# Optimization experiments

Measured on AMD Instinct MI355X. Metric: run time of the kernel, lower is better.

## Reference

```python
import jax, jax.numpy as jnp
import numpy as np

NUM_HEADS = 12
CF = 2            # compression_factor
DEPTH = 3
BLOCK_DEPTH = 2
TOTAL_DEPTH_M1 = 14 - 1


def setup_inputs() -> dict:
    key = jax.random.key(0)
    k1, k2, k3, k4 = jax.random.split(key, 4)
    B, N, C = 64, 577, 768
    x = jax.random.normal(k1, (B, N, C), dtype=jnp.float32)
    qkv_w = jax.random.normal(k2, (3 * C, C), dtype=jnp.float32) * (C ** -0.5)
    proj_w = jax.random.normal(k3, (C, C), dtype=jnp.float32) * (C ** -0.5)
    proj_b = jax.random.normal(k4, (C,), dtype=jnp.float32) * 0.02
    return {"x": x, "qkv_w": qkv_w, "proj_w": proj_w, "proj_b": proj_b}


def _attn_branch(xh, qkv_w, proj_w, proj_b, zero_small):
    Bh, N, C = xh.shape
    H = NUM_HEADS
    D = C // H
    scale = D ** -0.5
    # qkv projection (no bias), split into q,k,v of shape [Bh, H, N, D]
    qkv = jnp.einsum('bnc,oc->bno', xh, qkv_w)  # [Bh, N, 3C]
    qkv = qkv.reshape(Bh, N, 3, H, D).transpose(2, 0, 3, 1, 4)  # [3, Bh, H, N, D]
    if zero_small:
        # statically zero compressed heads in q, k, v (as the torch in-place write does)
        qkv = qkv.at[:, :, H // CF:].set(0.0)
    q, k, v = qkv[0], qkv[1], qkv[2]
    attn = jnp.einsum('bhnd,bhmd->bhnm', q, k) * scale
    attn = jax.nn.softmax(attn, axis=-1)
    out = jnp.einsum('bhnm,bhmd->bhnd', attn, v)
    out = out.transpose(0, 2, 1, 3).reshape(Bh, N, C)
    out = jnp.einsum('bnc,oc->bno', out, proj_w) + proj_b
    if zero_small:
        out = out.at[:, :, C // CF:].set(0.0)
    return out


def reference(x, qkv_w, proj_w, proj_b):
    B = x.shape[0]
    x_large = _attn_branch(x[:B // 2], qkv_w, proj_w, proj_b, zero_small=False)
    if BLOCK_DEPTH <= DEPTH <= TOTAL_DEPTH_M1 - BLOCK_DEPTH:
        x_small = _attn_branch(x[B // 2:], qkv_w, proj_w, proj_b, zero_small=True)
        return jnp.concatenate((x_large, x_small), axis=0)
    return jnp.concatenate((x_large, x_large), axis=0)
```

## Files before the change

### kernel.cpp

```cpp
#include <hip/hip_runtime.h>

#define BATCH 64
#define SEQ   577
#define CDIM  768
#define NH    12
#define HD    64
#define MROWS (BATCH * SEQ)
#define KDIM  768
#define QKV_N (3 * CDIM)
#define NPAD  640
#define TQ    128
#define PS    40
#define OS    72
#define DEAD_ROW0 18560

typedef short bf16x8 __attribute__((ext_vector_type(8)));
typedef float f32x4  __attribute__((ext_vector_type(4)));

__device__ __forceinline__ unsigned short f2bf(float f) {
  unsigned int u = __float_as_uint(f);
  u += 0x7fffu + ((u >> 16) & 1u);
  return (unsigned short)(u >> 16);
}

__device__ __forceinline__ void async_ld16(const unsigned short* g, unsigned short* l) {
  __builtin_amdgcn_global_load_lds((const __attribute__((address_space(1))) void*)g,
                                   (__attribute__((address_space(3))) void*)l, 16, 0, 0);
}

__global__ __launch_bounds__(256) void cvt_bf16(const float* __restrict__ in,
                                                unsigned short* __restrict__ out, int n4) {
  int i = blockIdx.x * 256 + threadIdx.x;
  if (i < n4) {
    float4 f = ((const float4*)in)[i];
    ushort4 o = make_ushort4(f2bf(f.x), f2bf(f.y), f2bf(f.z), f2bf(f.w));
    ((ushort4*)out)[i] = o;
  }
}

__global__ __launch_bounds__(256) void gemm_qkv(
    const unsigned short* __restrict__ A,
    const unsigned short* __restrict__ Bm,
    unsigned short* __restrict__ qb,
    unsigned short* __restrict__ kb,
    unsigned short* __restrict__ vb) {
  const int row0 = blockIdx.x * 128;
  const int col0 = blockIdx.y * 128;
  if (row0 >= DEAD_ROW0 && (col0 % CDIM) >= (CDIM / 2)) return;

  __shared__ unsigned short sA[128 * 32];
  __shared__ unsigned short sB[128 * 32];
  const int tid = threadIdx.x;
  const int w = tid >> 6, lane = tid & 63;
  const int quad = lane >> 4, l16 = lane & 15;
  const int wr = w >> 1, wc = w & 1;

  f32x4 acc[4][4] = {};

  for (int kt = 0; kt < KDIM; kt += 32) {
    __syncthreads();
    #pragma unroll
    for (int c = 0; c < 2; c++) {
      int i = tid + c * 256;
      int r = i >> 2, k8 = (i & 3) * 8;
      int ibase = (tid & ~63) + c * 256;
      int gr = row0 + r; if (gr >= MROWS) gr = MROWS - 1;
      async_ld16(A + gr * KDIM + kt + k8, sA + ibase * 8);
      int gc = col0 + r;
      async_ld16(Bm + gc * KDIM + kt + k8, sB + ibase * 8);
    }
    __syncthreads();

    bf16x8 af[4], bfv[4];
    #pragma unroll
    for (int i = 0; i < 4; i++)
      af[i] = *(const bf16x8*)&sA[(wr * 64 + i * 16 + l16) * 32 + quad * 8];
    #pragma unroll
    for (int j = 0; j < 4; j++)
      bfv[j] = *(const bf16x8*)&sB[(wc * 64 + j * 16 + l16) * 32 + quad * 8];
    #pragma unroll
    for (int i = 0; i < 4; i++)
      #pragma unroll
      for (int j = 0; j < 4; j++)
        acc[i][j] = __builtin_amdgcn_mfma_f32_16x16x32_bf16(af[i], bfv[j], acc[i][j], 0, 0, 0);
  }

  #pragma unroll
  for (int i = 0; i < 4; i++) {
    int mbase = row0 + wr * 64 + i * 16 + quad * 4;
    #pragma unroll
    for (int j = 0; j < 4; j++) {
      int col = col0 + wc * 64 + j * 16 + l16;
      int three = col / CDIM;
      int rem = col - three * CDIM;
      int h = rem >> 6, d = rem & 63;
      unsigned short* dst = (three == 0) ? qb : (three == 1) ? kb : vb;
      float sc = (three == 0) ? 0.180336878f : 1.0f;
      #pragma unroll
      for (int r = 0; r < 4; r++) {
        int m = mbase + r;
        if (m < MROWS) {
          int b = m / SEQ;
          int n = m - b * SEQ;
          dst[(((b * NH + h) * SEQ + n) << 6) + d] = f2bf(acc[i][j][r] * sc);
        }
      }
    }
  }
}

__global__ __launch_bounds__(512) void transpose_v(
    const unsigned short* __restrict__ v,
    unsigned short* __restrict__ vt) {
  const int bh = blockIdx.y;
  const int b = bh / NH, h = bh - b * NH;
  if (b >= 32 && h >= 6) return;
  const int t = blockIdx.x;
  const int tid = threadIdx.x;
  const int w = tid >> 6, lane = tid & 63;
  int n = t * 64 + lane;
  bf16x8 vv = {};
  if (n < SEQ)
    vv = *(const bf16x8*)&v[(size_t)bh * (SEQ * HD) + n * HD + w * 8];
  unsigned short* dst = vt + (size_t)bh * (HD * NPAD) + (w * 8) * NPAD + t * 64 + lane;
  #pragma unroll
  for (int j = 0; j < 8; j++)
    dst[j * NPAD] = ((const unsigned short*)&vv)[j];
}

__global__ __launch_bounds__(256, 4) void flash_attn(
    const unsigned short* __restrict__ q,
    const unsigned short* __restrict__ k,
    const unsigned short* __restrict__ vt,
    unsigned short* __restrict__ attn) {
  const int id = blockIdx.x;
  const int bh8 = id / 40;
  const int rem = id - bh8 * 40;
  const int qt = rem >> 3;
  const int bh = bh8 * 8 + (rem & 7);
  const int b = bh / NH, h = bh - b * NH;
  const int tid = threadIdx.x;
  const int w = tid >> 6, lane = tid & 63;
  const int quad = lane >> 4, l16 = lane & 15;

  if (b >= 32 && h >= 6) {
    for (int it = tid; it < TQ * 8; it += 256) {
      int r = it >> 3, c8 = (it & 7) * 8;
      int n = qt * TQ + r;
      if (n < SEQ)
        *(int4*)&attn[(b * SEQ + n) * CDIM + h * 64 + c8] = make_int4(0, 0, 0, 0);
    }
    return;
  }

  __shared__ unsigned short sK[2 * 64 * 32];
  __shared__ unsigned short sVt[2 * 64 * 32];
  __shared__ unsigned short sP[4][64 * PS];

  const unsigned short* qbase = q + (size_t)bh * (SEQ * HD);
  const unsigned short* kbase = k + (size_t)bh * (SEQ * HD);
  const unsigned short* vtbase = vt + (size_t)bh * (HD * NPAD);

  bf16x8 aq[2][2];
  #pragma unroll
  for (int g = 0; g < 2; g++) {
    int qr = qt * TQ + w * 32 + g * 16 + l16;
    if (qr > SEQ - 1) qr = SEQ - 1;
    aq[g][0] = *(const bf16x8*)&qbase[qr * HD + quad * 8];
    aq[g][1] = *(const bf16x8*)&qbase[qr * HD + 32 + quad * 8];
  }

  f32x4 oacc[2][4] = {};
  f32x4 lacc[2] = {};

  const short ONE = (short)0x3F80;

  for (int t = 0; t < 10; t++) {
    __syncthreads();
    #pragma unroll
    for (int c = 0; c < 2; c++) {
      int rI = tid >> 2, c4 = tid & 3;
      int base = c * 2048 + (tid & ~63) * 8;
      int kr = t * 64 + rI; if (kr > SEQ - 1) kr = SEQ - 1;
      async_ld16(kbase + kr * HD + c * 32 + c4 * 8, sK + base);
      async_ld16(vtbase + rI * NPAD + t * 64 + c * 32 + c4 * 8, sVt + base);
    }
    __syncthreads();

    bf16x8 bk[4][2];
    #pragma unroll
    for (int nt = 0; nt < 4; nt++) {
      bk[nt][0] = *(const bf16x8*)&sK[0 * 2048 + (nt * 16 + l16) * 32 + quad * 8];
      bk[nt][1] = *(const bf16x8*)&sK[1 * 2048 + (nt * 16 + l16) * 32 + quad * 8];
    }

    bf16x8 ones0, ones1;
    if (t < 9) {
      #pragma unroll
      for (int j = 0; j < 8; j++) { ones0[j] = ONE; ones1[j] = ONE; }
    } else {
      bf16x8 z = {};
      ones0 = z; ones1 = z;
      ones0[0] = (quad == 0) ? ONE : (short)0;
    }

    #pragma unroll
    for (int g = 0; g < 2; g++) {
      f32x4 s[4];
      #pragma unroll
      for (int nt = 0; nt < 4; nt++) {
        f32x4 z = {};
        z = __builtin_amdgcn_mfma_f32_16x16x32_bf16(aq[g][0], bk[nt][0], z, 0, 0, 0);
        z = __builtin_amdgcn_mfma_f32_16x16x32_bf16(aq[g][1], bk[nt][1], z, 0, 0, 0);
        s[nt] = z;
      }
      #pragma unroll
      for (int nt = 0; nt < 4; nt++)
        #pragma unroll
        for (int r = 0; r < 4; r++)
          sP[w][((g * 2 + (nt >> 1)) * 16 + quad * 4 + r) * PS + (nt & 1) * 16 + l16] =
              f2bf(__builtin_exp2f(s[nt][r]));
    }

    #pragma unroll
    for (int g = 0; g < 2; g++) {
      bf16x8 pa0 = *(const bf16x8*)&sP[w][((g * 2 + 0) * 16 + l16) * PS + quad * 8];
      bf16x8 pa1 = *(const bf16x8*)&sP[w][((g * 2 + 1) * 16 + l16) * PS + quad * 8];
      #pragma unroll
      for (int dt = 0; dt < 4; dt++) {
        bf16x8 bv0 = *(const bf16x8*)&sVt[0 * 2048 + (dt * 16 + l16) * 32 + quad * 8];
        bf16x8 bv1 = *(const bf16x8*)&sVt[1 * 2048 + (dt * 16 + l16) * 32 + quad * 8];
        oacc[g][dt] = __builtin_amdgcn_mfma_f32_16x16x32_bf16(pa0, bv0, oacc[g][dt], 0, 0, 0);
        oacc[g][dt] = __builtin_amdgcn_mfma_f32_16x16x32_bf16(pa1, bv1, oacc[g][dt], 0, 0, 0);
      }
      lacc[g] = __builtin_amdgcn_mfma_f32_16x16x32_bf16(pa0, ones0, lacc[g], 0, 0, 0);
      lacc[g] = __builtin_amdgcn_mfma_f32_16x16x32_bf16(pa1, ones1, lacc[g], 0, 0, 0);
    }
  }

  unsigned short* so = &sP[w][0];
  #pragma unroll
  for (int g = 0; g < 2; g++)
    #pragma unroll
    for (int r = 0; r < 4; r++) {
      float inv = 1.0f / lacc[g][r];
      #pragma unroll
      for (int dt = 0; dt < 4; dt++)
        so[(g * 16 + quad * 4 + r) * OS + dt * 16 + l16] = f2bf(oacc[g][dt][r] * inv);
    }
  #pragma unroll
  for (int it = 0; it < 4; it++) {
    int chunk = it * 64 + lane;
    int row = chunk >> 3, c8 = chunk & 7;
    int n = qt * TQ + w * 32 + row;
    if (n < SEQ)
      *(int4*)&attn[(b * SEQ + n) * CDIM + h * 64 + c8 * 8] =
          *(const int4*)&so[row * OS + c8 * 8];
  }
}

__global__ __launch_bounds__(256) void gemm_proj(
    const unsigned short* __restrict__ A,
    const unsigned short* __restrict__ Bm,
    const float* __restrict__ bias,
    float* __restrict__ out) {
  const int row0 = blockIdx.x * 128;
  const int col0 = blockIdx.y * 128;
  const int tid = threadIdx.x;

  if (row0 >= DEAD_ROW0 && col0 >= (CDIM / 2)) {
    float4 z4 = make_float4(0.f, 0.f, 0.f, 0.f);
    #pragma unroll
    for (int it = 0; it < 16; it++) {
      int idx = it * 256 + tid;
      int r = idx >> 5, c4 = idx & 31;
      int m = row0 + r;
      if (m < MROWS)
        *(float4*)&out[(size_t)m * CDIM + col0 + c4 * 4] = z4;
    }
    return;
  }

  __shared__ unsigned short sA[128 * 32];
  __shared__ unsigned short sB[128 * 32];
  const int w = tid >> 6, lane = tid & 63;
  const int quad = lane >> 4, l16 = lane & 15;
  const int wr = w >> 1, wc = w & 1;

  f32x4 acc[4][4] = {};

  for (int kt = 0; kt < KDIM; kt += 32) {
    __syncthreads();
    #pragma unroll
    for (int c = 0; c < 2; c++) {
      int i = tid + c * 256;
      int r = i >> 2, k8 = (i & 3) * 8;
      int ibase = (tid & ~63) + c * 256;
      int gr = row0 + r; if (gr >= MROWS) gr = MROWS - 1;
      async_ld16(A + gr * KDIM + kt + k8, sA + ibase * 8);
      int gc = col0 + r;
      async_ld16(Bm + gc * KDIM + kt + k8, sB + ibase * 8);
    }
    __syncthreads();

    bf16x8 af[4], bfv[4];
    #pragma unroll
    for (int i = 0; i < 4; i++)
      af[i] = *(const bf16x8*)&sA[(wr * 64 + i * 16 + l16) * 32 + quad * 8];
    #pragma unroll
    for (int j = 0; j < 4; j++)
      bfv[j] = *(const bf16x8*)&sB[(wc * 64 + j * 16 + l16) * 32 + quad * 8];
    #pragma unroll
    for (int i = 0; i < 4; i++)
      #pragma unroll
      for (int j = 0; j < 4; j++)
        acc[i][j] = __builtin_amdgcn_mfma_f32_16x16x32_bf16(af[i], bfv[j], acc[i][j], 0, 0, 0);
  }

  #pragma unroll
  for (int i = 0; i < 4; i++) {
    int mbase = row0 + wr * 64 + i * 16 + quad * 4;
    #pragma unroll
    for (int j = 0; j < 4; j++) {
      int col = col0 + wc * 64 + j * 16 + l16;
      float bv = bias[col];
      #pragma unroll
      for (int r = 0; r < 4; r++) {
        int m = mbase + r;
        if (m < MROWS) {
          int b = m / SEQ;
          float val = acc[i][j][r] + bv;
          if (b >= 32 && col >= (CDIM / 2)) val = 0.f;
          out[(size_t)m * CDIM + col] = val;
        }
      }
    }
  }
}

extern "C" void kernel_launch(void* const* d_in, const int* in_sizes, int n_in,
                              void* d_out, int out_size, void* d_ws, size_t ws_size,
                              hipStream_t stream) {
  const float* x      = (const float*)d_in[0];
  const float* qkv_w  = (const float*)d_in[1];
  const float* proj_w = (const float*)d_in[2];
  const float* proj_b = (const float*)d_in[3];
  float* out = (float*)d_out;

  size_t off = 0;
  auto alloc = [&](size_t bytes) {
    void* p = (char*)d_ws + off;
    off += (bytes + 255) & ~(size_t)255;
    return p;
  };
  const size_t XE = (size_t)MROWS * KDIM;
  unsigned short* xb   = (unsigned short*)alloc(XE * 2);
  unsigned short* wqb  = (unsigned short*)alloc((size_t)QKV_N * KDIM * 2);
  unsigned short* wpb  = (unsigned short*)alloc((size_t)CDIM * KDIM * 2);
  unsigned short* qb   = (unsigned short*)alloc(XE * 2);
  unsigned short* kb   = (unsigned short*)alloc(XE * 2);
  unsigned short* vb   = (unsigned short*)alloc(XE * 2);
  unsigned short* vtb  = (unsigned short*)alloc((size_t)BATCH * NH * HD * NPAD * 2);
  unsigned short* attnb = xb;
  (void)ws_size;

  cvt_bf16<<<(int)(XE / 4 / 256), 256, 0, stream>>>(x, xb, (int)(XE / 4));
  cvt_bf16<<<(QKV_N * KDIM / 4) / 256, 256, 0, stream>>>(qkv_w, wqb, QKV_N * KDIM / 4);
  cvt_bf16<<<(CDIM * KDIM / 4) / 256, 256, 0, stream>>>(proj_w, wpb, CDIM * KDIM / 4);

  gemm_qkv<<<dim3((MROWS + 127) / 128, QKV_N / 128), 256, 0, stream>>>(xb, wqb, qb, kb, vb);

  transpose_v<<<dim3(10, BATCH * NH), 512, 0, stream>>>(vb, vtb);

  flash_attn<<<(BATCH * NH / 8) * 40, 256, 0, stream>>>(qb, kb, vtb, attnb);

  gemm_proj<<<dim3((MROWS + 127) / 128, CDIM / 128), 256, 0, stream>>>(attnb, wpb, proj_b, out);
}
```

Measured before the change: 560.0 us.

## Rewrite QKV and projection GEMMs with 256x256 tiles and double-buffered LDS pipeline

Both GEMMs move from 128x128 tiles with 256 threads and a single LDS buffer to 256x256 tiles with 512 threads, a double-buffered 64-wide K pipeline, an XOR-swizzled LDS layout, MFMA priority boosts and XCD-aware block remapping. The QKV epilogue stages results through LDS so it can write 16-byte vectorized stores into the head-major q/k/v buffers. Dead-region skipping is now done per warp at finer granularity. The larger tiles raise data reuse and overlap loads with compute, at the cost of 128KB of LDS per block, fewer blocks per CU, and a coarser tail over 145x9 tiles.

```diff
diff --git a/kernel.cpp b/kernel.cpp
--- a/kernel.cpp
+++ b/kernel.cpp
@@ -12,7 +12,7 @@
 #define TQ    128
 #define PS    40
 #define OS    72
-#define DEAD_ROW0 18560
+#define DEAD_M 18464
 
 typedef short bf16x8 __attribute__((ext_vector_type(8)));
 typedef float f32x4  __attribute__((ext_vector_type(4)));
@@ -26,6 +26,13 @@
 __device__ __forceinline__ void async_ld16(const unsigned short* g, unsigned short* l) {
   __builtin_amdgcn_global_load_lds((const __attribute__((address_space(1))) void*)g,
                                    (__attribute__((address_space(3))) void*)l, 16, 0, 0);
+}
+
+__device__ __forceinline__ int xcd_swz(int id, int nwg) {
+  int q = nwg >> 3, r = nwg & 7;
+  int xcd = id & 7, lin = id >> 3;
+  int base = (xcd < r) ? xcd * (q + 1) : r * (q + 1) + (xcd - r) * q;
+  return base + lin;
 }
 
 __global__ __launch_bounds__(256) void cvt_bf16(const float* __restrict__ in,
@@ -38,73 +45,173 @@
   }
 }
 
-__global__ __launch_bounds__(256) void gemm_qkv(
+__device__ __forceinline__ void gemm256_loop(
+    const unsigned short* __restrict__ A,
+    const unsigned short* __restrict__ Bm,
+    unsigned short* sL,
+    int row0, int col0,
+    f32x4 (&acc)[8][4]) {
+  const int tid = threadIdx.x;
+  const int w = tid >> 6, lane = tid & 63;
+  const int quad = lane >> 4, l16 = lane & 15;
+  const int wm = w >> 2, wn = w & 3;
+
+  const int rl0 = w * 32 + (lane >> 2);
+  const int rl1 = rl0 + 16;
+  const int ch = (((lane & 3) ^ (rl0 & 3)) << 3);
+  int ga0 = row0 + rl0; if (ga0 >= MROWS) ga0 = MROWS - 1;
+  int ga1 = row0 + rl1; if (ga1 >= MROWS) ga1 = MROWS - 1;
+  const unsigned short* aSrc0 = A + (size_t)ga0 * KDIM + ch;
+  const unsigned short* aSrc1 = A + (size_t)ga1 * KDIM + ch;
+  const unsigned short* bSrc0 = Bm + (size_t)(col0 + rl0) * KDIM + ch;
+  const unsigned short* bSrc1 = Bm + (size_t)(col0 + rl1) * KDIM + ch;
+  const int sdst = w * 1024;
+
+  const int swz = ((quad ^ (l16 & 3)) << 3);
+  const int arow = (wm * 128 + l16) * 32 + swz;
+  const int brow = (wn * 64 + l16) * 32 + swz + 16384;
+
+#define STAGE_A(off, kt, ks) do {                                              \
+    async_ld16(aSrc0 + (kt) * 64 + (ks) * 32, sL + (off) + (ks) * 8192 + sdst);       \
+    async_ld16(aSrc1 + (kt) * 64 + (ks) * 32, sL + (off) + (ks) * 8192 + sdst + 512); \
+  } while (0)
+#define STAGE_B(off, kt, ks) do {                                              \
+    async_ld16(bSrc0 + (kt) * 64 + (ks) * 32, sL + (off) + 16384 + (ks) * 8192 + sdst);       \
+    async_ld16(bSrc1 + (kt) * 64 + (ks) * 32, sL + (off) + 16384 + (ks) * 8192 + sdst + 512); \
+  } while (0)
+
+  STAGE_A(0, 0, 0); STAGE_B(0, 0, 0); STAGE_A(0, 0, 1); STAGE_B(0, 0, 1);
+  asm volatile("s_waitcnt vmcnt(4)" ::: "memory");
+  __builtin_amdgcn_s_barrier();
+
+  bf16x8 af[8], bf[4];
+  #pragma unroll 2
+  for (int t = 0; t < 12; ++t) {
+    const int d = (t & 1) << 15;
+    const int nd = d ^ 32768;
+    const bool pre = (t < 11);
+    #pragma unroll
+    for (int mf = 0; mf < 8; ++mf)
+      af[mf] = *(const bf16x8*)&sL[d + arow + mf * 512];
+    bf[0] = *(const bf16x8*)&sL[d + brow];
+    bf[1] = *(const bf16x8*)&sL[d + brow + 512];
+    if (pre) STAGE_A(nd, t + 1, 0);
+    __builtin_amdgcn_s_barrier();
+    asm volatile("s_waitcnt lgkmcnt(0)" ::: "memory");
+    __builtin_amdgcn_sched_barrier(0);
+    __builtin_amdgcn_s_setprio(1);
+    #pragma unroll
+    for (int mf = 0; mf < 8; ++mf) {
+      acc[mf][0] = __builtin_amdgcn_mfma_f32_16x16x32_bf16(af[mf], bf[0], acc[mf][0], 0, 0, 0);
+      acc[mf][1] = __builtin_amdgcn_mfma_f32_16x16x32_bf16(af[mf], bf[1], acc[mf][1], 0, 0, 0);
+    }
+    __builtin_amdgcn_s_setprio(0);
+    __builtin_amdgcn_sched_barrier(0);
+    __builtin_amdgcn_s_barrier();
+    bf[2] = *(const bf16x8*)&sL[d + brow + 1024];
+    bf[3] = *(const bf16x8*)&sL[d + brow + 1536];
+    if (pre) STAGE_B(nd, t + 1, 0);
+    __builtin_amdgcn_s_barrier();
+    asm volatile("s_waitcnt lgkmcnt(0)" ::: "memory");
+    __builtin_amdgcn_sched_barrier(0);
+    __builtin_amdgcn_s_setprio(1);
+    #pragma unroll
+    for (int mf = 0; mf < 8; ++mf) {
+      acc[mf][2] = __builtin_amdgcn_mfma_f32_16x16x32_bf16(af[mf], bf[2], acc[mf][2], 0, 0, 0);
+      acc[mf][3] = __builtin_amdgcn_mfma_f32_16x16x32_bf16(af[mf], bf[3], acc[mf][3], 0, 0, 0);
+    }
+    __builtin_amdgcn_s_setprio(0);
+    __builtin_amdgcn_sched_barrier(0);
+    if (pre) asm volatile("s_waitcnt vmcnt(4)" ::: "memory");
+    else     asm volatile("s_waitcnt vmcnt(0)" ::: "memory");
+    __builtin_amdgcn_s_barrier();
+    #pragma unroll
+    for (int mf = 0; mf < 8; ++mf)
+      af[mf] = *(const bf16x8*)&sL[d + 8192 + arow + mf * 512];
+    bf[0] = *(const bf16x8*)&sL[d + 8192 + brow];
+    bf[1] = *(const bf16x8*)&sL[d + 8192 + brow + 512];
+    if (pre) STAGE_A(nd, t + 1, 1);
+    __builtin_amdgcn_s_barrier();
+    asm volatile("s_waitcnt lgkmcnt(0)" ::: "memory");
+    __builtin_amdgcn_sched_barrier(0);
+    __builtin_amdgcn_s_setprio(1);
+    #pragma unroll
+    for (int mf = 0; mf < 8; ++mf) {
+      acc[mf][0] = __builtin_amdgcn_mfma_f32_16x16x32_bf16(af[mf], bf[0], acc[mf][0], 0, 0, 0);
+      acc[mf][1] = __builtin_amdgcn_mfma_f32_16x16x32_bf16(af[mf], bf[1], acc[mf][1], 0, 0, 0);
+    }
+    __builtin_amdgcn_s_setprio(0);
+    __builtin_amdgcn_sched_barrier(0);
+    __builtin_amdgcn_s_barrier();
+    bf[2] = *(const bf16x8*)&sL[d + 8192 + brow + 1024];
+    bf[3] = *(const bf16x8*)&sL[d + 8192 + brow + 1536];
+    if (pre) STAGE_B(nd, t + 1, 1);
+    __builtin_amdgcn_s_barrier();
+    asm volatile("s_waitcnt lgkmcnt(0)" ::: "memory");
+    __builtin_amdgcn_sched_barrier(0);
+    __builtin_amdgcn_s_setprio(1);
+    #pragma unroll
+    for (int mf = 0; mf < 8; ++mf) {
+      acc[mf][2] = __builtin_amdgcn_mfma_f32_16x16x32_bf16(af[mf], bf[2], acc[mf][2], 0, 0, 0);
+      acc[mf][3] = __builtin_amdgcn_mfma_f32_16x16x32_bf16(af[mf], bf[3], acc[mf][3], 0, 0, 0);
+    }
+    __builtin_amdgcn_s_setprio(0);
+    __builtin_amdgcn_sched_barrier(0);
+    if (pre) asm volatile("s_waitcnt vmcnt(4)" ::: "memory");
+    __builtin_amdgcn_s_barrier();
+  }
+#undef STAGE_A
+#undef STAGE_B
+}
+
+__global__ __launch_bounds__(512, 2) void gemm_qkv(
     const unsigned short* __restrict__ A,
     const unsigned short* __restrict__ Bm,
     unsigned short* __restrict__ qb,
     unsigned short* __restrict__ kb,
     unsigned short* __restrict__ vb) {
-  const int row0 = blockIdx.x * 128;
-  const int col0 = blockIdx.y * 128;
-  if (row0 >= DEAD_ROW0 && (col0 % CDIM) >= (CDIM / 2)) return;
-
-  __shared__ unsigned short sA[128 * 32];
-  __shared__ unsigned short sB[128 * 32];
+  const int wg = xcd_swz(blockIdx.x, 145 * 9);
+  const int mt = wg / 9, nt = wg - mt * 9;
+  const int row0 = mt * 256, col0 = nt * 256;
+  if (row0 >= DEAD_M && (col0 % CDIM) == 512) return;
+
+  __shared__ unsigned short sL[65536];
+  f32x4 acc[8][4] = {};
+  gemm256_loop(A, Bm, sL, row0, col0, acc);
+
   const int tid = threadIdx.x;
   const int w = tid >> 6, lane = tid & 63;
   const int quad = lane >> 4, l16 = lane & 15;
-  const int wr = w >> 1, wc = w & 1;
-
-  f32x4 acc[4][4] = {};
-
-  for (int kt = 0; kt < KDIM; kt += 32) {
-    __syncthreads();
-    #pragma unroll
-    for (int c = 0; c < 2; c++) {
-      int i = tid + c * 256;
-      int r = i >> 2, k8 = (i & 3) * 8;
-      int ibase = (tid & ~63) + c * 256;
-      int gr = row0 + r; if (gr >= MROWS) gr = MROWS - 1;
-      async_ld16(A + gr * KDIM + kt + k8, sA + ibase * 8);
-      int gc = col0 + r;
-      async_ld16(Bm + gc * KDIM + kt + k8, sB + ibase * 8);
-    }
-    __syncthreads();
-
-    bf16x8 af[4], bfv[4];
-    #pragma unroll
-    for (int i = 0; i < 4; i++)
-      af[i] = *(const bf16x8*)&sA[(wr * 64 + i * 16 + l16) * 32 + quad * 8];
-    #pragma unroll
-    for (int j = 0; j < 4; j++)
-      bfv[j] = *(const bf16x8*)&sB[(wc * 64 + j * 16 + l16) * 32 + quad * 8];
-    #pragma unroll
-    for (int i = 0; i < 4; i++)
-      #pragma unroll
-      for (int j = 0; j < 4; j++)
-        acc[i][j] = __builtin_amdgcn_mfma_f32_16x16x32_bf16(af[i], bfv[j], acc[i][j], 0, 0, 0);
-  }
-
-  #pragma unroll
-  for (int i = 0; i < 4; i++) {
-    int mbase = row0 + wr * 64 + i * 16 + quad * 4;
-    #pragma unroll
-    for (int j = 0; j < 4; j++) {
-      int col = col0 + wc * 64 + j * 16 + l16;
-      int three = col / CDIM;
-      int rem = col - three * CDIM;
-      int h = rem >> 6, d = rem & 63;
-      unsigned short* dst = (three == 0) ? qb : (three == 1) ? kb : vb;
-      float sc = (three == 0) ? 0.180336878f : 1.0f;
-      #pragma unroll
-      for (int r = 0; r < 4; r++) {
-        int m = mbase + r;
-        if (m < MROWS) {
-          int b = m / SEQ;
-          int n = m - b * SEQ;
-          dst[(((b * NH + h) * SEQ + n) << 6) + d] = f2bf(acc[i][j][r] * sc);
-        }
+  const int wm = w >> 2, wn = w & 3;
+
+  const int wcol = col0 + wn * 64;
+  const int three = wcol / CDIM;
+  const int rem = wcol - three * CDIM;
+  const int h = rem >> 6;
+  unsigned short* dst = (three == 0) ? qb : (three == 1) ? kb : vb;
+  const float sc = (three == 0) ? 0.180336878f : 1.0f;
+  if ((row0 + wm * 128) >= DEAD_M && h >= 6) return;
+
+  unsigned short* so = sL + w * 8192;
+  #pragma unroll
+  for (int mf = 0; mf < 8; ++mf)
+    #pragma unroll
+    for (int nf = 0; nf < 4; ++nf)
+      #pragma unroll
+      for (int r = 0; r < 4; ++r) {
+        int rr = mf * 16 + quad * 4 + r;
+        so[rr * 64 + (((nf * 2 + (l16 >> 3)) ^ (rr & 7)) << 3) + (l16 & 7)] =
+            f2bf(acc[mf][nf][r] * sc);
       }
+  #pragma unroll
+  for (int it = 0; it < 16; ++it) {
+    int c = it * 64 + lane;
+    int rr = c >> 3, s8 = c & 7;
+    int m = row0 + wm * 128 + rr;
+    if (m < MROWS) {
+      int b = m / SEQ, n = m - b * SEQ;
+      *(int4*)&dst[((((size_t)b * NH + h) * SEQ + n) << 6) + s8 * 8] =
+          *(const int4*)&so[rr * 64 + ((s8 ^ (rr & 7)) << 3)];
     }
   }
 }
@@ -259,21 +366,22 @@
   }
 }
 
-__global__ __launch_bounds__(256) void gemm_proj(
+__global__ __launch_bounds__(512, 2) void gemm_proj(
     const unsigned short* __restrict__ A,
     const unsigned short* __restrict__ Bm,
     const float* __restrict__ bias,
     float* __restrict__ out) {
-  const int row0 = blockIdx.x * 128;
-  const int col0 = blockIdx.y * 128;
+  const int wg = xcd_swz(blockIdx.x, 145 * 3);
+  const int mt = wg / 3, nt = wg - mt * 3;
+  const int row0 = mt * 256, col0 = nt * 256;
   const int tid = threadIdx.x;
 
-  if (row0 >= DEAD_ROW0 && col0 >= (CDIM / 2)) {
+  if (row0 >= DEAD_M && col0 >= (CDIM / 2)) {
     float4 z4 = make_float4(0.f, 0.f, 0.f, 0.f);
     #pragma unroll
-    for (int it = 0; it < 16; it++) {
-      int idx = it * 256 + tid;
-      int r = idx >> 5, c4 = idx & 31;
+    for (int it = 0; it < 32; ++it) {
+      int idx = it * 512 + tid;
+      int r = idx >> 6, c4 = idx & 63;
       int m = row0 + r;
       if (m < MROWS)
         *(float4*)&out[(size_t)m * CDIM + col0 + c4 * 4] = z4;
@@ -281,56 +389,31 @@
     return;
   }
 
-  __shared__ unsigned short sA[128 * 32];
-  __shared__ unsigned short sB[128 * 32];
+  __shared__ unsigned short sL[65536];
+  f32x4 acc[8][4] = {};
+  gemm256_loop(A, Bm, sL, row0, col0, acc);
+
   const int w = tid >> 6, lane = tid & 63;
   const int quad = lane >> 4, l16 = lane & 15;
-  const int wr = w >> 1, wc = w & 1;
-
-  f32x4 acc[4][4] = {};
-
-  for (int kt = 0; kt < KDIM; kt += 32) {
-    __syncthreads();
-    #pragma unroll
-    for (int c = 0; c < 2; c++) {
-      int i = tid + c * 256;
-      int r = i >> 2, k8 = (i & 3) * 8;
-      int ibase = (tid & ~63) + c * 256;
-      int gr = row0 + r; if (gr >= MROWS) gr = MROWS - 1;
-      async_ld16(A + gr * KDIM + kt + k8, sA + ibase * 8);
-      int gc = col0 + r;
-      async_ld16(Bm + gc * KDIM + kt + k8, sB + ibase * 8);
-    }
-    __syncthreads();
-
-    bf16x8 af[4], bfv[4];
-    #pragma unroll
-    for (int i = 0; i < 4; i++)
-      af[i] = *(const bf16x8*)&sA[(wr * 64 + i * 16 + l16) * 32 + quad * 8];
-    #pragma unroll
-    for (int j = 0; j < 4; j++)
-      bfv[j] = *(const bf16x8*)&sB[(wc * 64 + j * 16 + l16) * 32 + quad * 8];
-    #pragma unroll
-    for (int i = 0; i < 4; i++)
-      #pragma unroll
-      for (int j = 0; j < 4; j++)
-        acc[i][j] = __builtin_amdgcn_mfma_f32_16x16x32_bf16(af[i], bfv[j], acc[i][j], 0, 0, 0);
-  }
-
-  #pragma unroll
-  for (int i = 0; i < 4; i++) {
-    int mbase = row0 + wr * 64 + i * 16 + quad * 4;
-    #pragma unroll
-    for (int j = 0; j < 4; j++) {
-      int col = col0 + wc * 64 + j * 16 + l16;
-      float bv = bias[col];
-      #pragma unroll
-      for (int r = 0; r < 4; r++) {
-        int m = mbase + r;
+  const int wm = w >> 2, wn = w & 3;
+
+  float bv[4];
+  #pragma unroll
+  for (int nf = 0; nf < 4; ++nf) bv[nf] = bias[col0 + wn * 64 + nf * 16 + l16];
+
+  #pragma unroll
+  for (int mf = 0; mf < 8; ++mf) {
+    int mb = row0 + wm * 128 + mf * 16 + quad * 4;
+    #pragma unroll
+    for (int nf = 0; nf < 4; ++nf) {
+      int col = col0 + wn * 64 + nf * 16 + l16;
+      bool maskc = (col >= (CDIM / 2));
+      #pragma unroll
+      for (int r = 0; r < 4; ++r) {
+        int m = mb + r;
         if (m < MROWS) {
-          int b = m / SEQ;
-          float val = acc[i][j][r] + bv;
-          if (b >= 32 && col >= (CDIM / 2)) val = 0.f;
+          float val = acc[mf][nf][r] + bv[nf];
+          if (m >= DEAD_M && maskc) val = 0.f;
           out[(size_t)m * CDIM + col] = val;
         }
       }
@@ -368,11 +451,11 @@
   cvt_bf16<<<(QKV_N * KDIM / 4) / 256, 256, 0, stream>>>(qkv_w, wqb, QKV_N * KDIM / 4);
   cvt_bf16<<<(CDIM * KDIM / 4) / 256, 256, 0, stream>>>(proj_w, wpb, CDIM * KDIM / 4);
 
-  gemm_qkv<<<dim3((MROWS + 127) / 128, QKV_N / 128), 256, 0, stream>>>(xb, wqb, qb, kb, vb);
+  gemm_qkv<<<dim3(145 * 9), 512, 0, stream>>>(xb, wqb, qb, kb, vb);
 
   transpose_v<<<dim3(10, BATCH * NH), 512, 0, stream>>>(vb, vtb);
 
   flash_attn<<<(BATCH * NH / 8) * 40, 256, 0, stream>>>(qb, kb, vtb, attnb);
 
-  gemm_proj<<<dim3((MROWS + 127) / 128, CDIM / 128), 256, 0, stream>>>(attnb, wpb, proj_b, out);
-}
+  gemm_proj<<<dim3(145 * 3), 512, 0, stream>>>(attnb, wpb, proj_b, out);
+}
```

Measured after the change: 557.6 us. No clear change (-0.4%).
